# Performance work log

Measured on AMD Instinct MI355X. Metric: run time of the kernel, lower is better.

## Reference

```python
import jax, jax.numpy as jnp
import numpy as np
from jax import lax

N_QUBITS = 4
DIM = 2 ** N_QUBITS  # 16-amplitude state vector


def _cnot_perm(c, t):
    # CNOT(control=c, target=t): amp_out[j] = amp_in[j ^ (bit_c(j) * mask_t)]
    idx = np.arange(DIM)
    mc = 1 << (N_QUBITS - 1 - c)  # PennyLane: wire 0 is most significant
    mt = 1 << (N_QUBITS - 1 - t)
    return jnp.asarray(np.where(idx & mc, idx ^ mt, idx))

# BasicEntanglerLayers ring pattern for n>2: CNOT(0,1),(1,2),(2,3),(3,0)
CNOT_PERMS = [_cnot_perm(i, (i + 1) % N_QUBITS) for i in range(N_QUBITS)]
_bits = (np.arange(DIM)[None, :] >> (N_QUBITS - 1 - np.arange(N_QUBITS)[:, None])) & 1
Z_SIGNS = jnp.asarray(1.0 - 2.0 * _bits, dtype=jnp.float32)  # [4,16], PauliZ eigenvalues


def _apply_1q(state, U, wire):
    # state: [B, 16] complex; U: [2,2] (shared) or [B,2,2] (per-sample angle)
    B = state.shape[0]
    s = state.reshape(B, 2 ** wire, 2, 2 ** (N_QUBITS - 1 - wire))
    if U.ndim == 2:
        s = jnp.einsum('ij,bajc->baic', U, s)
    else:
        s = jnp.einsum('bij,bajc->baic', U, s)
    return s.reshape(B, DIM)


def quantum_circuit(inputs, weights):
    # Batched default.qubit simulation. inputs: [B,4] angles, weights: [3,4].
    B = inputs.shape[0]
    state = jnp.zeros((B, DIM), jnp.complex64).at[:, 0].set(1.0)
    # RY(inputs[:,w]) on each wire (per-sample angles)
    for w in range(N_QUBITS):
        th = inputs[:, w] * 0.5
        c = jnp.cos(th).astype(jnp.complex64)
        s = jnp.sin(th).astype(jnp.complex64)
        U = jnp.stack([jnp.stack([c, -s], -1), jnp.stack([s, c], -1)], -2)  # [B,2,2]
        state = _apply_1q(state, U, w)
    # BasicEntanglerLayers: per layer, RX(weights[l,w]) on each wire then CNOT ring
    for l in range(weights.shape[0]):
        for w in range(N_QUBITS):
            th = weights[l, w] * 0.5
            cc = jnp.cos(th).astype(jnp.complex64)
            ss = (-1j) * jnp.sin(th).astype(jnp.complex64)
            U = jnp.stack([jnp.stack([cc, ss]), jnp.stack([ss, cc])])  # [2,2]
            state = _apply_1q(state, U, w)
        for w in range(N_QUBITS):
            state = state[:, CNOT_PERMS[w]]
    probs = jnp.abs(state) ** 2  # [B,16]
    return (probs @ Z_SIGNS.T).astype(jnp.float32)  # [B,4] <Z_w>


def setup_inputs() -> dict:
    key = jax.random.key(0)
    ks = jax.random.split(key, 8)
    B = 16384
    return {
        'x': jax.random.normal(ks[0], (B, 3, 32, 32), jnp.float32),
        'conv_w': jax.random.normal(ks[1], (N_QUBITS, 3, 3, 3), jnp.float32) * 0.1,
        'conv_b': jnp.zeros((N_QUBITS,), jnp.float32),
        'q_weights': jax.random.normal(ks[2], (3, N_QUBITS), jnp.float32),
        'w1': jax.random.normal(ks[3], (128, N_QUBITS), jnp.float32) * 0.1,
        'b1': jnp.zeros((128,), jnp.float32),
        'w2': jax.random.normal(ks[4], (3 * 32 * 32, 128), jnp.float32) * 0.05,
        'b2': jnp.zeros((3 * 32 * 32,), jnp.float32),
    }


def reference(x, conv_w, conv_b, q_weights, w1, b1, w2, b2):
    # Conv2d(3, 4, k=3, pad=1)
    y = lax.conv_general_dilated(
        x, conv_w, window_strides=(1, 1), padding='SAME',
        dimension_numbers=('NCHW', 'OIHW', 'NCHW')) + conv_b[None, :, None, None]
    # adaptive_avg_pool2d to (1,1) == global mean over H,W -> [B,4]
    pooled = y.mean(axis=(2, 3))
    # per-sample quantum circuit, batched; torch.tensor() in the original
    # detaches gradients, mirrored by stop_gradient
    q = lax.stop_gradient(quantum_circuit(pooled, q_weights))
    h = jax.nn.relu(q @ w1.T + b1)
    out = h @ w2.T + b2
    return out.reshape(-1, 3, 32, 32)
```

## Files before the change

### kernel.cpp

```cpp
#include <hip/hip_runtime.h>
#include <hip/hip_bf16.h>

typedef __attribute__((ext_vector_type(8))) short bf16x8;
typedef __attribute__((ext_vector_type(4))) float f32x4;

__device__ __forceinline__ unsigned short f2bf(float f) {
  union { __hip_bfloat16 b; unsigned short u; } cv;
  cv.b = __float2bfloat16(f);
  return cv.u;
}

__global__ __launch_bounds__(256) void k_cvt_w2(const float* __restrict__ w2,
                                                unsigned short* __restrict__ w2b) {
  const int i = (blockIdx.x * 256 + threadIdx.x) * 4;
  float4 v = *(const float4*)(w2 + i);
  union { uint2 u; unsigned short s[4]; } p;
  p.s[0] = f2bf(v.x); p.s[1] = f2bf(v.y); p.s[2] = f2bf(v.z); p.s[3] = f2bf(v.w);
  *(uint2*)(w2b + i) = p.u;
}

__global__ __launch_bounds__(256) void k_convpool(const float* __restrict__ x,
                                                  const float* __restrict__ cw,
                                                  const float* __restrict__ cb,
                                                  float* __restrict__ pooled) {
  const int wv = threadIdx.x >> 6;
  const int b = blockIdx.x * 4 + wv;
  const int t = threadIdx.x & 63;
  const float4* x4 = (const float4*)x + (size_t)b * 768;
  float F[3] = {0,0,0}, R0[3] = {0,0,0}, R31[3] = {0,0,0}, C0[3] = {0,0,0}, C31[3] = {0,0,0};
  float k00[3] = {0,0,0}, k031[3] = {0,0,0}, k310[3] = {0,0,0}, k3131[3] = {0,0,0};
#pragma unroll
  for (int g = 0; g < 12; ++g) {
    const int i = g >> 2;
    const int p = (g & 3) * 64 + t;
    const int h = p >> 3;
    const int wq = p & 7;
    float4 f = x4[g * 64 + t];
    float sm = f.x + f.y + f.z + f.w;
    F[i] += sm;
    if (h == 0)  R0[i]  += sm;
    if (h == 31) R31[i] += sm;
    if (wq == 0) C0[i]  += f.x;
    if (wq == 7) C31[i] += f.w;
    if (p == 0)   k00[i]   = f.x;
    if (p == 7)   k031[i]  = f.w;
    if (p == 248) k310[i]  = f.x;
    if (p == 255) k3131[i] = f.w;
  }
#pragma unroll
  for (int i = 0; i < 3; ++i) {
#pragma unroll
    for (int off = 32; off; off >>= 1) {
      F[i]   += __shfl_xor(F[i], off);
      R0[i]  += __shfl_xor(R0[i], off);
      R31[i] += __shfl_xor(R31[i], off);
      C0[i]  += __shfl_xor(C0[i], off);
      C31[i] += __shfl_xor(C31[i], off);
    }
    k00[i]   = __shfl(k00[i], 0);
    k031[i]  = __shfl(k031[i], 7);
    k310[i]  = __shfl(k310[i], 56);
    k3131[i] = __shfl(k3131[i], 63);
  }
  if (t < 4) {
    const int o = t;
    float acc = 0.f;
#pragma unroll
    for (int i = 0; i < 3; ++i) {
      const float* wp = cw + (o * 3 + i) * 9;
      float w00 = wp[0], w01 = wp[1], w02 = wp[2];
      float w10 = wp[3], w11 = wp[4], w12 = wp[5];
      float w20 = wp[6], w21 = wp[7], w22 = wp[8];
      acc += (w00 + w01 + w02 + w10 + w11 + w12 + w20 + w21 + w22) * F[i];
      acc -= (w20 + w21 + w22) * R0[i];
      acc -= (w00 + w01 + w02) * R31[i];
      acc -= (w02 + w12 + w22) * C0[i];
      acc -= (w00 + w10 + w20) * C31[i];
      acc += w00 * k3131[i] + w02 * k310[i] + w20 * k031[i] + w22 * k00[i];
    }
    pooled[b * 4 + o] = cb[o] + acc * (1.0f / 1024.0f);
  }
}

__global__ __launch_bounds__(64) void k_qnn(const float* __restrict__ pooled,
                                            const float* __restrict__ qw,
                                            const float* __restrict__ w1,
                                            const float* __restrict__ b1,
                                            unsigned short* __restrict__ hout) {
  const int b = blockIdx.x * 64 + threadIdx.x;
  float4 pv = *((const float4*)pooled + b);
  float c[4], s[4];
  {
    float th[4] = {pv.x * 0.5f, pv.y * 0.5f, pv.z * 0.5f, pv.w * 0.5f};
#pragma unroll
    for (int w = 0; w < 4; ++w) { s[w] = sinf(th[w]); c[w] = cosf(th[w]); }
  }
  float sr[16], si[16];
#pragma unroll
  for (int k = 0; k < 16; ++k) {
    sr[k] = (k & 8 ? s[0] : c[0]) * (k & 4 ? s[1] : c[1]) *
            (k & 2 ? s[2] : c[2]) * (k & 1 ? s[3] : c[3]);
    si[k] = 0.f;
  }
#pragma unroll
  for (int l = 0; l < 3; ++l) {
#pragma unroll
    for (int w = 0; w < 4; ++w) {
      float th = qw[l * 4 + w] * 0.5f;
      float cc = cosf(th), ss = sinf(th);
      const int m = 1 << (3 - w);
#pragma unroll
      for (int k = 0; k < 16; ++k) {
        if (!(k & m)) {
          const int kb = k | m;
          float ar = sr[k], ai = si[k], br = sr[kb], bi = si[kb];
          sr[k]  = cc * ar + ss * bi;
          si[k]  = cc * ai - ss * br;
          sr[kb] = cc * br + ss * ai;
          si[kb] = cc * bi - ss * ar;
        }
      }
    }
#pragma unroll
    for (int w = 0; w < 4; ++w) {
      const int mc = 1 << (3 - w);
      const int mt = 1 << (3 - ((w + 1) & 3));
#pragma unroll
      for (int k = 0; k < 16; ++k) {
        if ((k & mc) && !(k & mt)) {
          const int kb = k | mt;
          float tr = sr[k]; sr[k] = sr[kb]; sr[kb] = tr;
          float ti = si[k]; si[k] = si[kb]; si[kb] = ti;
        }
      }
    }
  }
  float q[4] = {0.f, 0.f, 0.f, 0.f};
#pragma unroll
  for (int k = 0; k < 16; ++k) {
    float pr = sr[k] * sr[k] + si[k] * si[k];
#pragma unroll
    for (int w = 0; w < 4; ++w) q[w] += (k & (1 << (3 - w))) ? -pr : pr;
  }
#pragma unroll 1
  for (int jb = 0; jb < 16; ++jb) {
    union { uint4 u; unsigned short us[8]; } pack;
#pragma unroll
    for (int jj = 0; jj < 8; ++jj) {
      const int j = jb * 8 + jj;
      float4 wv = *((const float4*)w1 + j);
      float hv = b1[j] + wv.x * q[0] + wv.y * q[1] + wv.z * q[2] + wv.w * q[3];
      pack.us[jj] = f2bf(fmaxf(hv, 0.f));
    }
    ((uint4*)hout)[b * 16 + jb] = pack.u;
  }
}

__global__ __launch_bounds__(256) void k_gemm(const unsigned short* __restrict__ hA,
                                              const unsigned short* __restrict__ w2b,
                                              const float* __restrict__ b2,
                                              float* __restrict__ out) {
  const int bn = blockIdx.x * 64;
  const int bm = blockIdx.y * 64;
  const int t = threadIdx.x;
  const int lane = t & 63, wv = t >> 6;
  __shared__ unsigned short As[64][136];
  __shared__ unsigned short Bs[64][136];
  for (int cch = t; cch < 1024; cch += 256) {
    const int r = cch >> 4;
    const int col8 = (cch & 15) * 8;
    uint4 va = *(const uint4*)(hA + (size_t)(bm + r) * 128 + col8);
    *(uint4*)(&As[r][col8]) = va;
    uint4 vb = *(const uint4*)(w2b + (size_t)(bn + r) * 128 + col8);
    *(uint4*)(&Bs[r][col8]) = vb;
  }
  __syncthreads();
  f32x4 acc[4] = {{0,0,0,0},{0,0,0,0},{0,0,0,0},{0,0,0,0}};
  const int mr = wv * 16 + (lane & 15);
  const int kq = (lane >> 4) * 8;
#pragma unroll
  for (int ks = 0; ks < 4; ++ks) {
    bf16x8 hfrag = *(const bf16x8*)(&As[mr][ks * 32 + kq]);
#pragma unroll
    for (int n = 0; n < 4; ++n) {
      bf16x8 wfrag = *(const bf16x8*)(&Bs[n * 16 + (lane & 15)][ks * 32 + kq]);
      acc[n] = __builtin_amdgcn_mfma_f32_16x16x32_bf16(wfrag, hfrag, acc[n], 0, 0, 0);
    }
  }
  const int m = bm + wv * 16 + (lane & 15);
  const int nq = (lane >> 4) << 2;
#pragma unroll
  for (int n = 0; n < 4; ++n) {
    const int n0 = bn + n * 16 + nq;
    float4 bias = *(const float4*)(b2 + n0);
    float4 o;
    o.x = acc[n][0] + bias.x;
    o.y = acc[n][1] + bias.y;
    o.z = acc[n][2] + bias.z;
    o.w = acc[n][3] + bias.w;
    *(float4*)(out + (size_t)m * 3072 + n0) = o;
  }
}

extern "C" void kernel_launch(void* const* d_in, const int* in_sizes, int n_in,
                              void* d_out, int out_size, void* d_ws, size_t ws_size,
                              hipStream_t stream) {
  const float* x      = (const float*)d_in[0];
  const float* conv_w = (const float*)d_in[1];
  const float* conv_b = (const float*)d_in[2];
  const float* qw     = (const float*)d_in[3];
  const float* w1     = (const float*)d_in[4];
  const float* b1     = (const float*)d_in[5];
  const float* w2     = (const float*)d_in[6];
  const float* b2     = (const float*)d_in[7];
  float* out = (float*)d_out;

  const int B = in_sizes[0] / 3072;

  char* ws = (char*)d_ws;
  float* pooled        = (float*)ws;
  unsigned short* hbf  = (unsigned short*)(ws + (size_t)B * 16);
  unsigned short* w2b  = (unsigned short*)(ws + (size_t)B * 16 + (size_t)B * 256);

  hipLaunchKernelGGL(k_cvt_w2, dim3(384), dim3(256), 0, stream, w2, w2b);
  hipLaunchKernelGGL(k_convpool, dim3(B / 4), dim3(256), 0, stream, x, conv_w, conv_b, pooled);
  hipLaunchKernelGGL(k_qnn, dim3(B / 64), dim3(64), 0, stream, pooled, qw, w1, b1, hbf);
  hipLaunchKernelGGL(k_gemm, dim3(48, B / 64), dim3(256), 0, stream, hbf, w2b, b2, out);
}
```

Before: 393.0 us.

## Fuse conv-pool and quantum circuit kernels, computing per-sample circuit per wavefront

Merges the conv+pool kernel with the quantum-circuit/MLP kernel so pooled values never round-trip through global memory and one launch is removed. Each wavefront handles one sample: the four pooled outputs are broadcast via shuffles, every lane redundantly simulates the 16-amplitude circuit, then each lane computes two of the 128 hidden units and writes them packed as bf16. This trades redundant per-lane circuit math (64x duplication) for coalesced hidden-layer writes and one fewer kernel.

```diff
diff --git a/kernel.cpp b/kernel.cpp
--- a/kernel.cpp
+++ b/kernel.cpp
@@ -19,10 +19,13 @@
   *(uint2*)(w2b + i) = p.u;
 }
 
-__global__ __launch_bounds__(256) void k_convpool(const float* __restrict__ x,
-                                                  const float* __restrict__ cw,
-                                                  const float* __restrict__ cb,
-                                                  float* __restrict__ pooled) {
+__global__ __launch_bounds__(256) void k_convqnn(const float* __restrict__ x,
+                                                 const float* __restrict__ cw,
+                                                 const float* __restrict__ cb,
+                                                 const float* __restrict__ qw,
+                                                 const float* __restrict__ w1,
+                                                 const float* __restrict__ b1,
+                                                 unsigned int* __restrict__ hout) {
   const int wv = threadIdx.x >> 6;
   const int b = blockIdx.x * 4 + wv;
   const int t = threadIdx.x & 63;
@@ -62,8 +65,9 @@
     k310[i]  = __shfl(k310[i], 56);
     k3131[i] = __shfl(k3131[i], 63);
   }
-  if (t < 4) {
-    const int o = t;
+  float pooled_o = 0.f;
+  {
+    const int o = t & 3;
     float acc = 0.f;
 #pragma unroll
     for (int i = 0; i < 3; ++i) {
@@ -78,22 +82,13 @@
       acc -= (w00 + w10 + w20) * C31[i];
       acc += w00 * k3131[i] + w02 * k310[i] + w20 * k031[i] + w22 * k00[i];
     }
-    pooled[b * 4 + o] = cb[o] + acc * (1.0f / 1024.0f);
-  }
-}
-
-__global__ __launch_bounds__(64) void k_qnn(const float* __restrict__ pooled,
-                                            const float* __restrict__ qw,
-                                            const float* __restrict__ w1,
-                                            const float* __restrict__ b1,
-                                            unsigned short* __restrict__ hout) {
-  const int b = blockIdx.x * 64 + threadIdx.x;
-  float4 pv = *((const float4*)pooled + b);
+    pooled_o = cb[o] + acc * (1.0f / 1024.0f);
+  }
   float c[4], s[4];
-  {
-    float th[4] = {pv.x * 0.5f, pv.y * 0.5f, pv.z * 0.5f, pv.w * 0.5f};
-#pragma unroll
-    for (int w = 0; w < 4; ++w) { s[w] = sinf(th[w]); c[w] = cosf(th[w]); }
+#pragma unroll
+  for (int w = 0; w < 4; ++w) {
+    float th = __shfl(pooled_o, w) * 0.5f;
+    s[w] = sinf(th); c[w] = cosf(th);
   }
   float sr[16], si[16];
 #pragma unroll
@@ -142,18 +137,15 @@
 #pragma unroll
     for (int w = 0; w < 4; ++w) q[w] += (k & (1 << (3 - w))) ? -pr : pr;
   }
-#pragma unroll 1
-  for (int jb = 0; jb < 16; ++jb) {
-    union { uint4 u; unsigned short us[8]; } pack;
-#pragma unroll
-    for (int jj = 0; jj < 8; ++jj) {
-      const int j = jb * 8 + jj;
-      float4 wv = *((const float4*)w1 + j);
-      float hv = b1[j] + wv.x * q[0] + wv.y * q[1] + wv.z * q[2] + wv.w * q[3];
-      pack.us[jj] = f2bf(fmaxf(hv, 0.f));
-    }
-    ((uint4*)hout)[b * 16 + jb] = pack.u;
-  }
+  const int j0 = 2 * t;
+  float4 wv0 = *((const float4*)w1 + j0);
+  float4 wv1 = *((const float4*)w1 + j0 + 1);
+  float2 bb = *((const float2*)(b1 + j0));
+  float h0 = bb.x + wv0.x * q[0] + wv0.y * q[1] + wv0.z * q[2] + wv0.w * q[3];
+  float h1 = bb.y + wv1.x * q[0] + wv1.y * q[1] + wv1.z * q[2] + wv1.w * q[3];
+  unsigned int packed = (unsigned int)f2bf(fmaxf(h0, 0.f)) |
+                        ((unsigned int)f2bf(fmaxf(h1, 0.f)) << 16);
+  hout[(size_t)b * 64 + t] = packed;
 }
 
 __global__ __launch_bounds__(256) void k_gemm(const unsigned short* __restrict__ hA,
@@ -218,12 +210,11 @@
   const int B = in_sizes[0] / 3072;
 
   char* ws = (char*)d_ws;
-  float* pooled        = (float*)ws;
-  unsigned short* hbf  = (unsigned short*)(ws + (size_t)B * 16);
-  unsigned short* w2b  = (unsigned short*)(ws + (size_t)B * 16 + (size_t)B * 256);
+  unsigned short* hbf  = (unsigned short*)ws;
+  unsigned short* w2b  = (unsigned short*)(ws + (size_t)B * 256);
 
   hipLaunchKernelGGL(k_cvt_w2, dim3(384), dim3(256), 0, stream, w2, w2b);
-  hipLaunchKernelGGL(k_convpool, dim3(B / 4), dim3(256), 0, stream, x, conv_w, conv_b, pooled);
-  hipLaunchKernelGGL(k_qnn, dim3(B / 64), dim3(64), 0, stream, pooled, qw, w1, b1, hbf);
+  hipLaunchKernelGGL(k_convqnn, dim3(B / 4), dim3(256), 0, stream,
+                     x, conv_w, conv_b, qw, w1, b1, (unsigned int*)hbf);
   hipLaunchKernelGGL(k_gemm, dim3(48, B / 64), dim3(256), 0, stream, hbf, w2b, b2, out);
 }
```

After: 404.2 us. +2.9%, slower.
